# Optimization experiments

Hardware: AMD Instinct MI355X
Metric: run time of the kernel (lower is better)

## Reference

```python
import jax, jax.numpy as jnp
import numpy as np

B, Q, K, A, H, C, O = 32, 512, 512, 256, 8, 32, 256  # batch, queries, keys, channels, heads, head_dim, out_dim


def setup_inputs() -> dict:
    key = jax.random.key(0)
    ks = jax.random.split(key, 12)
    s = 0.02
    return {
        "q_data": jax.random.normal(ks[0], (B, Q, A), jnp.float32),
        "m_data": jax.random.normal(ks[1], (B, K, A), jnp.float32),
        "bias": jax.random.normal(ks[2], (B, 1, 1, K), jnp.float32),
        "nonbatched_bias": jax.random.normal(ks[3], (H, Q, K), jnp.float32),
        "batched_bias": jax.random.normal(ks[4], (B, H, Q, K), jnp.float32),
        "query_w": jax.random.normal(ks[5], (A, H, C), jnp.float32) * s,
        "key_w": jax.random.normal(ks[6], (A, H, C), jnp.float32) * s,
        "value_w": jax.random.normal(ks[7], (A, H, C), jnp.float32) * s,
        "gating_w": jax.random.normal(ks[8], (A, H, C), jnp.float32) * s,
        "gating_b": jnp.ones((H, C), jnp.float32),
        "output_w": jax.random.normal(ks[9], (H, C, O), jnp.float32) * s,
        "output_b": jnp.zeros((O,), jnp.float32),
    }


def reference(q_data, m_data, bias, nonbatched_bias, batched_bias,
              query_w, key_w, value_w, gating_w, gating_b, output_w, output_b):
    key_scale = query_w.shape[-1] ** -0.5
    q = jnp.einsum('bqa,ahc->bqhc', q_data, query_w) * key_scale
    k = jnp.einsum('bka,ahc->bkhc', m_data, key_w)
    v = jnp.einsum('bka,ahc->bkhc', m_data, value_w)
    logits = jnp.einsum('bqhc,bkhc->bhqk', q, k) + bias
    logits = logits + nonbatched_bias[None] + batched_bias
    weights = jax.nn.softmax(logits, axis=-1)
    weighted_avg = jnp.einsum('bhqk,bkhc->bqhc', weights, v)
    gate = jax.nn.sigmoid(jnp.einsum('bqc,chv->bqhv', q_data, gating_w) + gating_b)
    weighted_avg = weighted_avg * gate
    return jnp.einsum('bqhc,hco->bqo', weighted_avg, output_w) + output_b
```

## Files before the change

### kernel.cpp

```cpp
#include <hip/hip_runtime.h>
#include <cstdint>
#include <cstddef>


typedef __attribute__((ext_vector_type(8))) short short8;
typedef __attribute__((ext_vector_type(4))) float f32x4;
typedef __attribute__((ext_vector_type(4))) unsigned int u32x4;
typedef __attribute__((ext_vector_type(2))) unsigned int u32x2;

#define DEVFN static __device__ __forceinline__
#define L2E 1.4426950408889634f

DEVFN unsigned short f2b(float f) {
  unsigned int u = __builtin_bit_cast(unsigned int, f);
  u += 0x7fffu + ((u >> 16) & 1u);
  return (unsigned short)(u >> 16);
}
DEVFN float b2f(unsigned int bits16) {
  return __builtin_bit_cast(float, bits16 << 16);
}
DEVFN unsigned int pack2(float a, float b) {
  return (unsigned int)f2b(a) | ((unsigned int)f2b(b) << 16);
}
DEVFN f32x4 mfma16(short8 a, short8 b, f32x4 c) {
  return __builtin_amdgcn_mfma_f32_16x16x32_bf16(a, b, c, 0, 0, 0);
}

__global__ __launch_bounds__(256) void wtrans_kernel(
    const float* __restrict__ qw, const float* __restrict__ kw,
    const float* __restrict__ vw, const float* __restrict__ gw,
    const float* __restrict__ ow,
    unsigned short* __restrict__ wtq, unsigned short* __restrict__ wtk,
    unsigned short* __restrict__ wtv, unsigned short* __restrict__ wtg,
    unsigned short* __restrict__ wt3)
{
  const int matid = blockIdx.x >> 4;
  const int tile  = blockIdx.x & 15;
  const float* src = (matid == 0) ? qw : (matid == 1) ? kw : (matid == 2) ? vw
                   : (matid == 3) ? gw : ow;
  unsigned short* dst = (matid == 0) ? wtq : (matid == 1) ? wtk : (matid == 2) ? wtv
                      : (matid == 3) ? wtg : wt3;
  const int tr = (tile >> 2) * 64, tc = (tile & 3) * 64;
  __shared__ unsigned short T[64 * 72];
  const int t = threadIdx.x;
  {
    const int row = t >> 2, cb = (t & 3) * 16;
#pragma unroll
    for (int ii = 0; ii < 4; ++ii) {
      f32x4 v = *(const f32x4*)&src[(size_t)(tr + row) * 256 + tc + cb + ii * 4];
      u32x2 p; p.x = pack2(v.x, v.y); p.y = pack2(v.z, v.w);
      *(u32x2*)&T[row * 72 + cb + ii * 4] = p;
    }
  }
  __syncthreads();
  {
    const int c0 = t >> 2, rb = (t & 3) * 16;
    unsigned short vals[16];
#pragma unroll
    for (int m = 0; m < 16; ++m) vals[m] = T[(rb + m) * 72 + c0];
    u32x4 s0, s1;
    s0.x = (unsigned)vals[0]  | ((unsigned)vals[1]  << 16);
    s0.y = (unsigned)vals[2]  | ((unsigned)vals[3]  << 16);
    s0.z = (unsigned)vals[4]  | ((unsigned)vals[5]  << 16);
    s0.w = (unsigned)vals[6]  | ((unsigned)vals[7]  << 16);
    s1.x = (unsigned)vals[8]  | ((unsigned)vals[9]  << 16);
    s1.y = (unsigned)vals[10] | ((unsigned)vals[11] << 16);
    s1.z = (unsigned)vals[12] | ((unsigned)vals[13] << 16);
    s1.w = (unsigned)vals[14] | ((unsigned)vals[15] << 16);
    unsigned short* dp = &dst[(size_t)(tc + c0) * 256 + tr + rb];
    *(u32x4*)dp = s0;
    *(u32x4*)(dp + 8) = s1;
  }
}

__global__ __launch_bounds__(256, 2) void proj_kernel(
    const float* __restrict__ q_data, const float* __restrict__ m_data,
    const unsigned short* __restrict__ wtq, const unsigned short* __restrict__ wtk,
    const unsigned short* __restrict__ wtv, const unsigned short* __restrict__ wtg,
    const float* __restrict__ gating_b,
    unsigned short* __restrict__ qp, unsigned short* __restrict__ kp,
    unsigned short* __restrict__ vp, float* __restrict__ gate)
{
  const int bid = blockIdx.x;
  const bool mside = bid >= 256;
  const int r0 = (mside ? bid - 256 : bid) * 64;
  const float* inp = mside ? m_data : q_data;
  __shared__ unsigned short Alds[64 * 264];
  __shared__ unsigned short Wlds[2][256 * 40];
  const int t = threadIdx.x;
  const int lane = t & 63, wave = t >> 6;
  const int l15 = lane & 15, g = lane >> 4;

  {
    const int row = t >> 2, cb = (t & 3) * 64;
    const float* ip = &inp[(size_t)(r0 + row) * 256 + cb];
#pragma unroll
    for (int i = 0; i < 8; ++i) {
      f32x4 a0 = *(const f32x4*)&ip[i * 8];
      f32x4 a1 = *(const f32x4*)&ip[i * 8 + 4];
      u32x4 pk;
      pk.x = pack2(a0.x, a0.y); pk.y = pack2(a0.z, a0.w);
      pk.z = pack2(a1.x, a1.y); pk.w = pack2(a1.z, a1.w);
      *(u32x4*)&Alds[row * 264 + cb + i * 8] = pk;
    }
  }

  const unsigned short* wt0 = mside ? wtk : wtq;
  const unsigned short* wt1 = mside ? wtv : wtg;

  {
    const u32x4* wsrc = (const u32x4*)&wt0[(size_t)t * 256];
    u32x4 a = wsrc[0], b = wsrc[1], c = wsrc[2], d = wsrc[3];
    *(u32x4*)&Wlds[0][t * 40 + 0]  = a;
    *(u32x4*)&Wlds[0][t * 40 + 8]  = b;
    *(u32x4*)&Wlds[0][t * 40 + 16] = c;
    *(u32x4*)&Wlds[0][t * 40 + 24] = d;
  }

  f32x4 acc[16];
#pragma unroll
  for (int nt = 0; nt < 16; ++nt) acc[nt] = f32x4{0.f, 0.f, 0.f, 0.f};

  const int arow = (wave * 16 + l15) * 264 + 8 * g;
  const int grow = r0 + wave * 16 + l15;
  const int ob = grow >> 9, oq = grow & 511;

#pragma unroll
  for (int s = 0; s < 16; ++s) {
    const int p = s & 1;
    __syncthreads();
    u32x4 nw0, nw1, nw2, nw3;
    if (s < 15) {
      const unsigned short* wt = (s + 1 < 8) ? wt0 : wt1;
      const u32x4* wsrc = (const u32x4*)&wt[(size_t)t * 256 + ((s + 1) & 7) * 32];
      nw0 = wsrc[0]; nw1 = wsrc[1]; nw2 = wsrc[2]; nw3 = wsrc[3];
    }
    const int ks = s & 7;
    short8 bf = __builtin_bit_cast(short8, *(const u32x4*)&Alds[arow + ks * 32]);
#pragma unroll
    for (int nt = 0; nt < 16; ++nt) {
      short8 wf = __builtin_bit_cast(short8,
          *(const u32x4*)&Wlds[p][(nt * 16 + l15) * 40 + 8 * g]);
      acc[nt] = mfma16(wf, bf, acc[nt]);
    }
    if (s < 15) {
      *(u32x4*)&Wlds[p ^ 1][t * 40 + 0]  = nw0;
      *(u32x4*)&Wlds[p ^ 1][t * 40 + 8]  = nw1;
      *(u32x4*)&Wlds[p ^ 1][t * 40 + 16] = nw2;
      *(u32x4*)&Wlds[p ^ 1][t * 40 + 24] = nw3;
    }
    if (s == 7 || s == 15) {
      const int oi = s >> 3;
#pragma unroll
      for (int nt = 0; nt < 16; ++nt) {
        const int n0 = nt * 16 + 4 * g;
        const int h = n0 >> 5, c0 = n0 & 31;
        const size_t idx = ((size_t)(ob * 8 + h) * 512 + oq) * 32 + c0;
        f32x4 v = acc[nt];
        if (!mside) {
          if (oi == 0) {
            u32x2 st;
            st.x = pack2(v.x * 0.17677669529663687f, v.y * 0.17677669529663687f);
            st.y = pack2(v.z * 0.17677669529663687f, v.w * 0.17677669529663687f);
            *(u32x2*)&qp[idx] = st;
          } else {
            f32x4 gb = *(const f32x4*)&gating_b[n0];
            f32x4 gv;
            gv.x = 1.0f / (1.0f + exp2f(-(v.x + gb.x) * L2E));
            gv.y = 1.0f / (1.0f + exp2f(-(v.y + gb.y) * L2E));
            gv.z = 1.0f / (1.0f + exp2f(-(v.z + gb.z) * L2E));
            gv.w = 1.0f / (1.0f + exp2f(-(v.w + gb.w) * L2E));
            *(f32x4*)&gate[idx] = gv;
          }
        } else {
          u32x2 st;
          st.x = pack2(v.x, v.y); st.y = pack2(v.z, v.w);
          if (oi == 0) *(u32x2*)&kp[idx] = st;
          else         *(u32x2*)&vp[idx] = st;
        }
        acc[nt] = f32x4{0.f, 0.f, 0.f, 0.f};
      }
    }
  }
}

__global__ __launch_bounds__(512, 4) void attn_kernel(
    const unsigned short* __restrict__ qp, const unsigned short* __restrict__ kp,
    const unsigned short* __restrict__ vp,
    const float* __restrict__ bias, const float* __restrict__ nbias,
    const float* __restrict__ bbias,
    unsigned short* __restrict__ wa)
{
  const int bid = blockIdx.x;
  const int h = bid & 7;
  const int qh = (bid >> 3) & 1;
  const int b = bid >> 4;
  const int bh = b * 8 + h;
  const int t = threadIdx.x;
  const int lane = t & 63, wave = t >> 6;
  const int l15 = lane & 15, g = lane >> 4;

  __shared__ unsigned short Klds[512 * 40];
  __shared__ unsigned short Vt[32 * 520];

  {
    const int row = t;
    const u32x4* ks = (const u32x4*)&kp[((size_t)bh * 512 + row) * 32];
    u32x4 k0 = ks[0], k1 = ks[1], k2 = ks[2], k3 = ks[3];
    *(u32x4*)&Klds[row * 40 + 0]  = k0;
    *(u32x4*)&Klds[row * 40 + 8]  = k1;
    *(u32x4*)&Klds[row * 40 + 16] = k2;
    *(u32x4*)&Klds[row * 40 + 24] = k3;
    const u32x4* vs = (const u32x4*)&vp[((size_t)bh * 512 + row) * 32];
#pragma unroll
    for (int cc = 0; cc < 4; ++cc) {
      u32x4 vv = vs[cc];
      unsigned int dw0 = vv.x, dw1 = vv.y, dw2 = vv.z, dw3 = vv.w;
      const int c = cc * 8;
      Vt[(c + 0) * 520 + row] = (unsigned short)(dw0 & 0xffff);
      Vt[(c + 1) * 520 + row] = (unsigned short)(dw0 >> 16);
      Vt[(c + 2) * 520 + row] = (unsigned short)(dw1 & 0xffff);
      Vt[(c + 3) * 520 + row] = (unsigned short)(dw1 >> 16);
      Vt[(c + 4) * 520 + row] = (unsigned short)(dw2 & 0xffff);
      Vt[(c + 5) * 520 + row] = (unsigned short)(dw2 >> 16);
      Vt[(c + 6) * 520 + row] = (unsigned short)(dw3 & 0xffff);
      Vt[(c + 7) * 520 + row] = (unsigned short)(dw3 >> 16);
    }
  }

  const int qbase = qh * 256 + wave * 32;
  short8 qf[2];
#pragma unroll
  for (int qt = 0; qt < 2; ++qt)
    qf[qt] = __builtin_bit_cast(short8,
        *(const u32x4*)&qp[((size_t)bh * 512 + qbase + qt * 16 + l15) * 32 + 8 * g]);

  const float* bbp = bbias + (size_t)bh * 512 * 512;
  const float* nbp = nbias + (size_t)h * 512 * 512;
  const float* bkp = bias + (size_t)b * 512;

  f32x4 acc[2][2];
#pragma unroll
  for (int ct = 0; ct < 2; ++ct)
#pragma unroll
    for (int qt = 0; qt < 2; ++qt) acc[ct][qt] = f32x4{0.f, 0.f, 0.f, 0.f};
  float l_r[2] = {0.f, 0.f};

  __syncthreads();

  const int pib = ((g & 1) << 4) | ((g >> 1) << 3);
  const bool godd = (g & 1) != 0;

  for (int kt = 0; kt < 16; ++kt) {
    const int k0 = kt * 32;
    short8 kf0 = __builtin_bit_cast(short8, *(const u32x4*)&Klds[(k0 + l15) * 40 + 8 * g]);
    short8 kf1 = __builtin_bit_cast(short8, *(const u32x4*)&Klds[(k0 + 16 + l15) * 40 + 8 * g]);
    short8 vf0 = __builtin_bit_cast(short8, *(const u32x4*)&Vt[l15 * 520 + k0 + pib]);
    short8 vf1 = __builtin_bit_cast(short8, *(const u32x4*)&Vt[(16 + l15) * 520 + k0 + pib]);
    f32x4 bk0 = *(const f32x4*)&bkp[k0 + 4 * g];
    f32x4 bk1 = *(const f32x4*)&bkp[k0 + 16 + 4 * g];
#pragma unroll
    for (int qt = 0; qt < 2; ++qt) {
      const int q = qbase + qt * 16 + l15;
      const float* bq = &bbp[(size_t)q * 512 + k0 + 4 * g];
      const float* nq = &nbp[(size_t)q * 512 + k0 + 4 * g];
      f32x4 bb0 = *(const f32x4*)bq;
      f32x4 bb1 = *(const f32x4*)(bq + 16);
      f32x4 nb0 = *(const f32x4*)nq;
      f32x4 nb1 = *(const f32x4*)(nq + 16);
      const f32x4 z = {0.f, 0.f, 0.f, 0.f};
      f32x4 s0 = mfma16(kf0, qf[qt], z);
      f32x4 s1 = mfma16(kf1, qf[qt], z);
      s0 = s0 + bb0 + nb0 + bk0;
      s1 = s1 + bb1 + nb1 + bk1;
      f32x4 p0, p1;
      p0.x = exp2f(s0.x * L2E); p0.y = exp2f(s0.y * L2E);
      p0.z = exp2f(s0.z * L2E); p0.w = exp2f(s0.w * L2E);
      p1.x = exp2f(s1.x * L2E); p1.y = exp2f(s1.y * L2E);
      p1.z = exp2f(s1.z * L2E); p1.w = exp2f(s1.w * L2E);
      float sum8 = (p0.x + p0.y) + (p0.z + p0.w) + (p1.x + p1.y) + (p1.z + p1.w);
      sum8 += __shfl_xor(sum8, 16, 64);
      sum8 += __shfl_xor(sum8, 32, 64);
      l_r[qt] += sum8;
      unsigned int d0 = pack2(p0.x, p0.y), d1 = pack2(p0.z, p0.w);
      unsigned int e0 = pack2(p1.x, p1.y), e1 = pack2(p1.z, p1.w);
      unsigned int pd0 = __shfl_xor(d0, 16, 64), pd1 = __shfl_xor(d1, 16, 64);
      unsigned int pe0 = __shfl_xor(e0, 16, 64), pe1 = __shfl_xor(e1, 16, 64);
      u32x4 pfu;
      pfu.x = godd ? pe0 : d0;
      pfu.y = godd ? pe1 : d1;
      pfu.z = godd ? e0 : pd0;
      pfu.w = godd ? e1 : pd1;
      short8 pf = __builtin_bit_cast(short8, pfu);
      acc[0][qt] = mfma16(vf0, pf, acc[0][qt]);
      acc[1][qt] = mfma16(vf1, pf, acc[1][qt]);
    }
  }

  unsigned short* wab = wa + (size_t)bh * 512 * 32;
#pragma unroll
  for (int qt = 0; qt < 2; ++qt) {
    const float rl = 1.0f / l_r[qt];
    const int q = qbase + qt * 16 + l15;
#pragma unroll
    for (int ct = 0; ct < 2; ++ct) {
      f32x4 v = acc[ct][qt];
      u32x2 st;
      st.x = pack2(v.x * rl, v.y * rl);
      st.y = pack2(v.z * rl, v.w * rl);
      *(u32x2*)&wab[q * 32 + ct * 16 + 4 * g] = st;
    }
  }
}

__global__ __launch_bounds__(256, 2) void outp_kernel(
    const unsigned short* __restrict__ wa, const float* __restrict__ gate,
    const unsigned short* __restrict__ wt3, const float* __restrict__ out_b,
    float* __restrict__ out)
{
  const int r0 = blockIdx.x * 64;
  const int t = threadIdx.x;
  const int lane = t & 63, wave = t >> 6;
  const int l15 = lane & 15, g = lane >> 4;
  __shared__ unsigned short Wlds[2][256 * 40];

  const int grow = r0 + wave * 16 + l15;
  const int b = grow >> 9, q = grow & 511;

  {
    const u32x4* wsrc = (const u32x4*)&wt3[(size_t)t * 256];
    u32x4 a = wsrc[0], bb = wsrc[1], c = wsrc[2], d = wsrc[3];
    *(u32x4*)&Wlds[0][t * 40 + 0]  = a;
    *(u32x4*)&Wlds[0][t * 40 + 8]  = bb;
    *(u32x4*)&Wlds[0][t * 40 + 16] = c;
    *(u32x4*)&Wlds[0][t * 40 + 24] = d;
  }
  size_t aidx = ((size_t)(b * 8 + 0) * 512 + q) * 32 + 8 * g;
  u32x4 cwv = *(const u32x4*)&wa[aidx];
  f32x4 cg0 = *(const f32x4*)&gate[aidx];
  f32x4 cg1 = *(const f32x4*)&gate[aidx + 4];

  f32x4 acc[16];
#pragma unroll
  for (int nt = 0; nt < 16; ++nt) acc[nt] = f32x4{0.f, 0.f, 0.f, 0.f};

#pragma unroll
  for (int s = 0; s < 8; ++s) {
    const int p = s & 1;
    __syncthreads();
    u32x4 nw0, nw1, nw2, nw3, nwv;
    f32x4 ng0, ng1;
    if (s < 7) {
      const u32x4* wsrc = (const u32x4*)&wt3[(size_t)t * 256 + (s + 1) * 32];
      nw0 = wsrc[0]; nw1 = wsrc[1]; nw2 = wsrc[2]; nw3 = wsrc[3];
      const size_t na = ((size_t)(b * 8 + s + 1) * 512 + q) * 32 + 8 * g;
      nwv = *(const u32x4*)&wa[na];
      ng0 = *(const f32x4*)&gate[na];
      ng1 = *(const f32x4*)&gate[na + 4];
    }
    float f0 = b2f(cwv.x & 0xffff) * cg0.x, f1 = b2f(cwv.x >> 16) * cg0.y;
    float f2 = b2f(cwv.y & 0xffff) * cg0.z, f3 = b2f(cwv.y >> 16) * cg0.w;
    float f4 = b2f(cwv.z & 0xffff) * cg1.x, f5 = b2f(cwv.z >> 16) * cg1.y;
    float f6 = b2f(cwv.w & 0xffff) * cg1.z, f7 = b2f(cwv.w >> 16) * cg1.w;
    u32x4 au;
    au.x = pack2(f0, f1); au.y = pack2(f2, f3);
    au.z = pack2(f4, f5); au.w = pack2(f6, f7);
    short8 af = __builtin_bit_cast(short8, au);
#pragma unroll
    for (int nt = 0; nt < 16; ++nt) {
      short8 wf = __builtin_bit_cast(short8,
          *(const u32x4*)&Wlds[p][(nt * 16 + l15) * 40 + 8 * g]);
      acc[nt] = mfma16(wf, af, acc[nt]);
    }
    if (s < 7) {
      *(u32x4*)&Wlds[p ^ 1][t * 40 + 0]  = nw0;
      *(u32x4*)&Wlds[p ^ 1][t * 40 + 8]  = nw1;
      *(u32x4*)&Wlds[p ^ 1][t * 40 + 16] = nw2;
      *(u32x4*)&Wlds[p ^ 1][t * 40 + 24] = nw3;
      cwv = nwv; cg0 = ng0; cg1 = ng1;
    }
  }
#pragma unroll
  for (int nt = 0; nt < 16; ++nt) {
    const int o0 = nt * 16 + 4 * g;
    f32x4 ob4 = *(const f32x4*)&out_b[o0];
    f32x4 v = acc[nt] + ob4;
    *(f32x4*)&out[(size_t)grow * 256 + o0] = v;
  }
}

extern "C" void kernel_launch(void* const* d_in, const int* in_sizes, int n_in,
                              void* d_out, int out_size, void* d_ws, size_t ws_size,
                              hipStream_t stream)
{
  const float* q_data   = (const float*)d_in[0];
  const float* m_data   = (const float*)d_in[1];
  const float* bias     = (const float*)d_in[2];
  const float* nbb      = (const float*)d_in[3];
  const float* bbb      = (const float*)d_in[4];
  const float* query_w  = (const float*)d_in[5];
  const float* key_w    = (const float*)d_in[6];
  const float* value_w  = (const float*)d_in[7];
  const float* gating_w = (const float*)d_in[8];
  const float* gating_b = (const float*)d_in[9];
  const float* output_w = (const float*)d_in[10];
  const float* output_b = (const float*)d_in[11];
  float* out = (float*)d_out;

  const size_t QP_B   = (size_t)32 * 8 * 512 * 32 * 2;
  const size_t GATE_B = (size_t)32 * 8 * 512 * 32 * 4;
  const size_t WT_B   = (size_t)256 * 256 * 2;

  char* ws = (char*)d_ws;
  unsigned short* qp  = (unsigned short*)(ws);
  unsigned short* kp  = (unsigned short*)(ws + QP_B);
  unsigned short* vp  = (unsigned short*)(ws + 2 * QP_B);
  unsigned short* wab = (unsigned short*)(ws + 3 * QP_B);
  float*          gat = (float*)(ws + 4 * QP_B);
  unsigned short* wtq = (unsigned short*)(ws + 4 * QP_B + GATE_B);
  unsigned short* wtk = (unsigned short*)(ws + 4 * QP_B + GATE_B + WT_B);
  unsigned short* wtv = (unsigned short*)(ws + 4 * QP_B + GATE_B + 2 * WT_B);
  unsigned short* wtg = (unsigned short*)(ws + 4 * QP_B + GATE_B + 3 * WT_B);
  unsigned short* wt3 = (unsigned short*)(ws + 4 * QP_B + GATE_B + 4 * WT_B);
  const size_t need = 4 * QP_B + GATE_B + 5 * WT_B;
  if (ws_size < need) return;

  hipLaunchKernelGGL(wtrans_kernel, dim3(80), dim3(256), 0, stream,
                     query_w, key_w, value_w, gating_w, output_w,
                     wtq, wtk, wtv, wtg, wt3);
  hipLaunchKernelGGL(proj_kernel, dim3(512), dim3(256), 0, stream,
                     q_data, m_data, wtq, wtk, wtv, wtg, gating_b,
                     qp, kp, vp, gat);
  hipLaunchKernelGGL(attn_kernel, dim3(512), dim3(512), 0, stream,
                     qp, kp, vp, bias, nbb, bbb, wab);
  hipLaunchKernelGGL(outp_kernel, dim3(256), dim3(256), 0, stream,
                     wab, gat, wt3, output_b, out);
}
```

Before: 137.5 us.

## Store gate in bf16, split projection N-tiles across waves, fold bias into MFMA

The projection kernel now runs 512 threads per block, with each wave covering half of the output columns. This halves the accumulator registers per thread and raises occupancy. The gate tensor is stored as bf16 instead of fp32, which halves its write and read traffic between the projection and output kernels at some cost in precision. The output kernel uses 32-row blocks split across waves by column half, giving twice as many blocks. The attention kernel passes the summed biases as the MFMA accumulator input instead of adding them after the MFMA.

```diff
diff --git a/kernel.cpp b/kernel.cpp
--- a/kernel.cpp
+++ b/kernel.cpp
@@ -73,13 +73,13 @@
   }
 }
 
-__global__ __launch_bounds__(256, 2) void proj_kernel(
+__global__ __launch_bounds__(512, 4) void proj_kernel(
     const float* __restrict__ q_data, const float* __restrict__ m_data,
     const unsigned short* __restrict__ wtq, const unsigned short* __restrict__ wtk,
     const unsigned short* __restrict__ wtv, const unsigned short* __restrict__ wtg,
     const float* __restrict__ gating_b,
     unsigned short* __restrict__ qp, unsigned short* __restrict__ kp,
-    unsigned short* __restrict__ vp, float* __restrict__ gate)
+    unsigned short* __restrict__ vp, unsigned short* __restrict__ gate)
 {
   const int bid = blockIdx.x;
   const bool mside = bid >= 256;
@@ -90,12 +90,13 @@
   const int t = threadIdx.x;
   const int lane = t & 63, wave = t >> 6;
   const int l15 = lane & 15, g = lane >> 4;
-
-  {
-    const int row = t >> 2, cb = (t & 3) * 64;
+  const int stripe = wave & 3, nhalf = wave >> 2;
+
+  {
+    const int row = t >> 3, cb = (t & 7) * 32;
     const float* ip = &inp[(size_t)(r0 + row) * 256 + cb];
 #pragma unroll
-    for (int i = 0; i < 8; ++i) {
+    for (int i = 0; i < 4; ++i) {
       f32x4 a0 = *(const f32x4*)&ip[i * 8];
       f32x4 a1 = *(const f32x4*)&ip[i * 8 + 4];
       u32x4 pk;
@@ -107,56 +108,54 @@
 
   const unsigned short* wt0 = mside ? wtk : wtq;
   const unsigned short* wt1 = mside ? wtv : wtg;
-
-  {
-    const u32x4* wsrc = (const u32x4*)&wt0[(size_t)t * 256];
-    u32x4 a = wsrc[0], b = wsrc[1], c = wsrc[2], d = wsrc[3];
-    *(u32x4*)&Wlds[0][t * 40 + 0]  = a;
-    *(u32x4*)&Wlds[0][t * 40 + 8]  = b;
-    *(u32x4*)&Wlds[0][t * 40 + 16] = c;
-    *(u32x4*)&Wlds[0][t * 40 + 24] = d;
-  }
-
-  f32x4 acc[16];
-#pragma unroll
-  for (int nt = 0; nt < 16; ++nt) acc[nt] = f32x4{0.f, 0.f, 0.f, 0.f};
-
-  const int arow = (wave * 16 + l15) * 264 + 8 * g;
-  const int grow = r0 + wave * 16 + l15;
+  const int wrow = t & 255, whalf = t >> 8;
+
+  {
+    const u32x4* wsrc = (const u32x4*)&wt0[(size_t)wrow * 256 + whalf * 16];
+    u32x4 a = wsrc[0], b = wsrc[1];
+    *(u32x4*)&Wlds[0][wrow * 40 + whalf * 16 + 0] = a;
+    *(u32x4*)&Wlds[0][wrow * 40 + whalf * 16 + 8] = b;
+  }
+
+  f32x4 acc[8];
+#pragma unroll
+  for (int j = 0; j < 8; ++j) acc[j] = f32x4{0.f, 0.f, 0.f, 0.f};
+
+  const int arow = (stripe * 16 + l15) * 264 + 8 * g;
+  const int grow = r0 + stripe * 16 + l15;
   const int ob = grow >> 9, oq = grow & 511;
 
 #pragma unroll
   for (int s = 0; s < 16; ++s) {
     const int p = s & 1;
     __syncthreads();
-    u32x4 nw0, nw1, nw2, nw3;
+    u32x4 nw0, nw1;
     if (s < 15) {
       const unsigned short* wt = (s + 1 < 8) ? wt0 : wt1;
-      const u32x4* wsrc = (const u32x4*)&wt[(size_t)t * 256 + ((s + 1) & 7) * 32];
-      nw0 = wsrc[0]; nw1 = wsrc[1]; nw2 = wsrc[2]; nw3 = wsrc[3];
+      const u32x4* wsrc =
+          (const u32x4*)&wt[(size_t)wrow * 256 + ((s + 1) & 7) * 32 + whalf * 16];
+      nw0 = wsrc[0]; nw1 = wsrc[1];
     }
     const int ks = s & 7;
     short8 bf = __builtin_bit_cast(short8, *(const u32x4*)&Alds[arow + ks * 32]);
 #pragma unroll
-    for (int nt = 0; nt < 16; ++nt) {
+    for (int j = 0; j < 8; ++j) {
       short8 wf = __builtin_bit_cast(short8,
-          *(const u32x4*)&Wlds[p][(nt * 16 + l15) * 40 + 8 * g]);
-      acc[nt] = mfma16(wf, bf, acc[nt]);
+          *(const u32x4*)&Wlds[p][((nhalf * 8 + j) * 16 + l15) * 40 + 8 * g]);
+      acc[j] = mfma16(wf, bf, acc[j]);
     }
     if (s < 15) {
-      *(u32x4*)&Wlds[p ^ 1][t * 40 + 0]  = nw0;
-      *(u32x4*)&Wlds[p ^ 1][t * 40 + 8]  = nw1;
-      *(u32x4*)&Wlds[p ^ 1][t * 40 + 16] = nw2;
-      *(u32x4*)&Wlds[p ^ 1][t * 40 + 24] = nw3;
+      *(u32x4*)&Wlds[p ^ 1][wrow * 40 + whalf * 16 + 0] = nw0;
+      *(u32x4*)&Wlds[p ^ 1][wrow * 40 + whalf * 16 + 8] = nw1;
     }
     if (s == 7 || s == 15) {
       const int oi = s >> 3;
 #pragma unroll
-      for (int nt = 0; nt < 16; ++nt) {
-        const int n0 = nt * 16 + 4 * g;
+      for (int j = 0; j < 8; ++j) {
+        const int n0 = (nhalf * 8 + j) * 16 + 4 * g;
         const int h = n0 >> 5, c0 = n0 & 31;
         const size_t idx = ((size_t)(ob * 8 + h) * 512 + oq) * 32 + c0;
-        f32x4 v = acc[nt];
+        f32x4 v = acc[j];
         if (!mside) {
           if (oi == 0) {
             u32x2 st;
@@ -170,7 +169,9 @@
             gv.y = 1.0f / (1.0f + exp2f(-(v.y + gb.y) * L2E));
             gv.z = 1.0f / (1.0f + exp2f(-(v.z + gb.z) * L2E));
             gv.w = 1.0f / (1.0f + exp2f(-(v.w + gb.w) * L2E));
-            *(f32x4*)&gate[idx] = gv;
+            u32x2 st;
+            st.x = pack2(gv.x, gv.y); st.y = pack2(gv.z, gv.w);
+            *(u32x2*)&gate[idx] = st;
           }
         } else {
           u32x2 st;
@@ -178,7 +179,7 @@
           if (oi == 0) *(u32x2*)&kp[idx] = st;
           else         *(u32x2*)&vp[idx] = st;
         }
-        acc[nt] = f32x4{0.f, 0.f, 0.f, 0.f};
+        acc[j] = f32x4{0.f, 0.f, 0.f, 0.f};
       }
     }
   }
@@ -268,11 +269,10 @@
       f32x4 bb1 = *(const f32x4*)(bq + 16);
       f32x4 nb0 = *(const f32x4*)nq;
       f32x4 nb1 = *(const f32x4*)(nq + 16);
-      const f32x4 z = {0.f, 0.f, 0.f, 0.f};
-      f32x4 s0 = mfma16(kf0, qf[qt], z);
-      f32x4 s1 = mfma16(kf1, qf[qt], z);
-      s0 = s0 + bb0 + nb0 + bk0;
-      s1 = s1 + bb1 + nb1 + bk1;
+      f32x4 c0 = (bb0 + nb0) + bk0;
+      f32x4 c1 = (bb1 + nb1) + bk1;
+      f32x4 s0 = mfma16(kf0, qf[qt], c0);
+      f32x4 s1 = mfma16(kf1, qf[qt], c1);
       f32x4 p0, p1;
       p0.x = exp2f(s0.x * L2E); p0.y = exp2f(s0.y * L2E);
       p0.z = exp2f(s0.z * L2E); p0.w = exp2f(s0.w * L2E);
@@ -314,17 +314,18 @@
 }
 
 __global__ __launch_bounds__(256, 2) void outp_kernel(
-    const unsigned short* __restrict__ wa, const float* __restrict__ gate,
+    const unsigned short* __restrict__ wa, const unsigned short* __restrict__ gate,
     const unsigned short* __restrict__ wt3, const float* __restrict__ out_b,
     float* __restrict__ out)
 {
-  const int r0 = blockIdx.x * 64;
+  const int r0 = blockIdx.x * 32;
   const int t = threadIdx.x;
   const int lane = t & 63, wave = t >> 6;
   const int l15 = lane & 15, g = lane >> 4;
+  const int stripe = wave & 1, half = wave >> 1;
   __shared__ unsigned short Wlds[2][256 * 40];
 
-  const int grow = r0 + wave * 16 + l15;
+  const int grow = r0 + stripe * 16 + l15;
   const int b = grow >> 9, q = grow & 511;
 
   {
@@ -337,54 +338,55 @@
   }
   size_t aidx = ((size_t)(b * 8 + 0) * 512 + q) * 32 + 8 * g;
   u32x4 cwv = *(const u32x4*)&wa[aidx];
-  f32x4 cg0 = *(const f32x4*)&gate[aidx];
-  f32x4 cg1 = *(const f32x4*)&gate[aidx + 4];
-
-  f32x4 acc[16];
-#pragma unroll
-  for (int nt = 0; nt < 16; ++nt) acc[nt] = f32x4{0.f, 0.f, 0.f, 0.f};
+  u32x4 cgv = *(const u32x4*)&gate[aidx];
+
+  f32x4 acc[8];
+#pragma unroll
+  for (int j = 0; j < 8; ++j) acc[j] = f32x4{0.f, 0.f, 0.f, 0.f};
 
 #pragma unroll
   for (int s = 0; s < 8; ++s) {
     const int p = s & 1;
     __syncthreads();
-    u32x4 nw0, nw1, nw2, nw3, nwv;
-    f32x4 ng0, ng1;
+    u32x4 nw0, nw1, nw2, nw3, nwv, ngv;
     if (s < 7) {
       const u32x4* wsrc = (const u32x4*)&wt3[(size_t)t * 256 + (s + 1) * 32];
       nw0 = wsrc[0]; nw1 = wsrc[1]; nw2 = wsrc[2]; nw3 = wsrc[3];
       const size_t na = ((size_t)(b * 8 + s + 1) * 512 + q) * 32 + 8 * g;
       nwv = *(const u32x4*)&wa[na];
-      ng0 = *(const f32x4*)&gate[na];
-      ng1 = *(const f32x4*)&gate[na + 4];
-    }
-    float f0 = b2f(cwv.x & 0xffff) * cg0.x, f1 = b2f(cwv.x >> 16) * cg0.y;
-    float f2 = b2f(cwv.y & 0xffff) * cg0.z, f3 = b2f(cwv.y >> 16) * cg0.w;
-    float f4 = b2f(cwv.z & 0xffff) * cg1.x, f5 = b2f(cwv.z >> 16) * cg1.y;
-    float f6 = b2f(cwv.w & 0xffff) * cg1.z, f7 = b2f(cwv.w >> 16) * cg1.w;
+      ngv = *(const u32x4*)&gate[na];
+    }
+    float f0 = b2f(cwv.x & 0xffff) * b2f(cgv.x & 0xffff);
+    float f1 = b2f(cwv.x >> 16)    * b2f(cgv.x >> 16);
+    float f2 = b2f(cwv.y & 0xffff) * b2f(cgv.y & 0xffff);
+    float f3 = b2f(cwv.y >> 16)    * b2f(cgv.y >> 16);
+    float f4 = b2f(cwv.z & 0xffff) * b2f(cgv.z & 0xffff);
+    float f5 = b2f(cwv.z >> 16)    * b2f(cgv.z >> 16);
+    float f6 = b2f(cwv.w & 0xffff) * b2f(cgv.w & 0xffff);
+    float f7 = b2f(cwv.w >> 16)    * b2f(cgv.w >> 16);
     u32x4 au;
     au.x = pack2(f0, f1); au.y = pack2(f2, f3);
     au.z = pack2(f4, f5); au.w = pack2(f6, f7);
     short8 af = __builtin_bit_cast(short8, au);
 #pragma unroll
-    for (int nt = 0; nt < 16; ++nt) {
+    for (int j = 0; j < 8; ++j) {
       short8 wf = __builtin_bit_cast(short8,
-          *(const u32x4*)&Wlds[p][(nt * 16 + l15) * 40 + 8 * g]);
-      acc[nt] = mfma16(wf, af, acc[nt]);
+          *(const u32x4*)&Wlds[p][((half * 8 + j) * 16 + l15) * 40 + 8 * g]);
+      acc[j] = mfma16(wf, af, acc[j]);
     }
     if (s < 7) {
       *(u32x4*)&Wlds[p ^ 1][t * 40 + 0]  = nw0;
       *(u32x4*)&Wlds[p ^ 1][t * 40 + 8]  = nw1;
       *(u32x4*)&Wlds[p ^ 1][t * 40 + 16] = nw2;
       *(u32x4*)&Wlds[p ^ 1][t * 40 + 24] = nw3;
-      cwv = nwv; cg0 = ng0; cg1 = ng1;
-    }
-  }
-#pragma unroll
-  for (int nt = 0; nt < 16; ++nt) {
-    const int o0 = nt * 16 + 4 * g;
+      cwv = nwv; cgv = ngv;
+    }
+  }
+#pragma unroll
+  for (int j = 0; j < 8; ++j) {
+    const int o0 = (half * 8 + j) * 16 + 4 * g;
     f32x4 ob4 = *(const f32x4*)&out_b[o0];
-    f32x4 v = acc[nt] + ob4;
+    f32x4 v = acc[j] + ob4;
     *(f32x4*)&out[(size_t)grow * 256 + o0] = v;
   }
 }
@@ -408,7 +410,7 @@
   float* out = (float*)d_out;
 
   const size_t QP_B   = (size_t)32 * 8 * 512 * 32 * 2;
-  const size_t GATE_B = (size_t)32 * 8 * 512 * 32 * 4;
+  const size_t GATE_B = (size_t)32 * 8 * 512 * 32 * 2;
   const size_t WT_B   = (size_t)256 * 256 * 2;
 
   char* ws = (char*)d_ws;
@@ -416,7 +418,7 @@
   unsigned short* kp  = (unsigned short*)(ws + QP_B);
   unsigned short* vp  = (unsigned short*)(ws + 2 * QP_B);
   unsigned short* wab = (unsigned short*)(ws + 3 * QP_B);
-  float*          gat = (float*)(ws + 4 * QP_B);
+  unsigned short* gat = (unsigned short*)(ws + 4 * QP_B);
   unsigned short* wtq = (unsigned short*)(ws + 4 * QP_B + GATE_B);
   unsigned short* wtk = (unsigned short*)(ws + 4 * QP_B + GATE_B + WT_B);
   unsigned short* wtv = (unsigned short*)(ws + 4 * QP_B + GATE_B + 2 * WT_B);
@@ -428,11 +430,11 @@
   hipLaunchKernelGGL(wtrans_kernel, dim3(80), dim3(256), 0, stream,
                      query_w, key_w, value_w, gating_w, output_w,
                      wtq, wtk, wtv, wtg, wt3);
-  hipLaunchKernelGGL(proj_kernel, dim3(512), dim3(256), 0, stream,
+  hipLaunchKernelGGL(proj_kernel, dim3(512), dim3(512), 0, stream,
                      q_data, m_data, wtq, wtk, wtv, wtg, gating_b,
                      qp, kp, vp, gat);
   hipLaunchKernelGGL(attn_kernel, dim3(512), dim3(512), 0, stream,
                      qp, kp, vp, bias, nbb, bbb, wab);
-  hipLaunchKernelGGL(outp_kernel, dim3(256), dim3(256), 0, stream,
+  hipLaunchKernelGGL(outp_kernel, dim3(512), dim3(256), 0, stream,
                      wab, gat, wt3, output_b, out);
 }
```

Result: no change. 135.7 us (-1.3%).
